# Kernel optimization log

Measured on AMD Instinct MI355X. Metric: run time of the kernel, lower is better.

Reference implementation:

```python
import jax, jax.numpy as jnp
import numpy as np

B, T, T_KEEP, C, F, K = 8, 128, 64, 128, 32, 64


def setup_inputs() -> dict:
    key = jax.random.key(0)
    k1, k2 = jax.random.split(key)
    y_true = jax.random.normal(k1, (B, T, C, F), dtype=jnp.float32)
    # per-timestep mask: 0 = keep, 1 = masked; constant over C,F and batch
    # (required by the original layer's Reshape using sum(1 - masktime[0]))
    masktime = jnp.concatenate([jnp.zeros((T_KEEP,), jnp.float32),
                                jnp.ones((T - T_KEEP,), jnp.float32)])
    mask = jnp.broadcast_to(masktime[None, :, None, None], (B, T, C, F)).astype(jnp.float32)
    centers = jax.random.normal(k2, (K,), dtype=jnp.float32)
    return {"y_true": y_true, "mask": mask, "centers": centers, "t_keep": T_KEEP}


def reference(y_true, mask, centers, t_keep):
    # masktime: [B, T]; mask is constant over channel/feature dims
    masktime = mask[:, :, 0, 0]
    # tf.boolean_mask keeps elements where (1 - mask) is True, preserving order.
    # Since mask is per-timestep, this is a gather of the unmasked timesteps.
    # Stable argsort puts zeros (kept timesteps) first, in original order.
    keep_idx = jnp.argsort(masktime[0], stable=True)[:t_keep]          # [T_keep]
    x = y_true[:, keep_idx]                                            # [B, T_keep, C, F]
    # element-wise nearest-center assignment (assign_center) + one-hot
    dist = jnp.abs(x[..., None] - centers)                             # [B, T_keep, C, F, K]
    idx = jnp.argmin(dist, axis=-1)                                    # [B, T_keep, C, F]
    return jax.nn.one_hot(idx, centers.shape[0], dtype=y_true.dtype)   # [B, T_keep, C, F, K]
```

## Files before the change

### kernel.cpp

```cpp
#include <hip/hip_runtime.h>

constexpr int B = 8, T = 128, T_KEEP = 64, C = 128, F = 32, K = 64;
constexpr int CF = C * F;
constexpr int TOTAL = B * T_KEEP * C * F;
constexpr int BLOCK = 256;
constexpr int EPT = 4;
constexpr int EPB = BLOCK * EPT;

typedef float vfloat4 __attribute__((ext_vector_type(4)));

__global__ void __launch_bounds__(BLOCK) assign_onehot_fused(
        const float* __restrict__ y,
        const float* __restrict__ mask,
        const float* __restrict__ centers,
        float* __restrict__ out) {
    __shared__ float sc[K];
    __shared__ float m_s[T];
    __shared__ int keep_s;
    const int tid = threadIdx.x;

    if (tid < K) sc[tid] = centers[tid];
    if (tid < T) m_s[tid] = mask[(size_t)tid * CF];
    __syncthreads();

    const int t_blk = (blockIdx.x >> 2) & (T_KEEP - 1);
    if (tid < T) {
        float mt = m_s[tid];
        int rank = 0;
        #pragma unroll 8
        for (int j = 0; j < T; ++j) {
            float mj = m_s[j];
            rank += (mj < mt) || (mj == mt && j < tid);
        }
        if (rank == t_blk) keep_s = tid;
    }
    __syncthreads();
    const int keep_t = keep_s;

    const int lane = tid & 63;
    const int wave = tid >> 6;
    const int wbase = blockIdx.x * EPB + wave * (EPT * 64);

    const int b   = wbase >> 18;
    const int cf0 = wbase & (CF - 1);
    const float* ysrc = y + (size_t)b * (T * CF) + (size_t)keep_t * CF + cf0;

    const float x0 = ysrc[lane];
    const float x1 = ysrc[64 + lane];
    const float x2 = ysrc[128 + lane];
    const float x3 = ysrc[192 + lane];

    int bi0 = 0, bi1 = 0, bi2 = 0, bi3 = 0;
    float bd0 = __builtin_inff(), bd1 = bd0, bd2 = bd0, bd3 = bd0;
    const float4* c4 = (const float4*)sc;
    #pragma unroll
    for (int k4 = 0; k4 < K / 4; ++k4) {
        float4 cv = c4[k4];
        float d;
        #define UPD(cvx, kk)                                            \
            d = fabsf(x0 - cvx); if (d < bd0) { bd0 = d; bi0 = kk; }    \
            d = fabsf(x1 - cvx); if (d < bd1) { bd1 = d; bi1 = kk; }    \
            d = fabsf(x2 - cvx); if (d < bd2) { bd2 = d; bi2 = kk; }    \
            d = fabsf(x3 - cvx); if (d < bd3) { bd3 = d; bi3 = kk; }
        UPD(cv.x, 4 * k4 + 0)
        UPD(cv.y, 4 * k4 + 1)
        UPD(cv.z, 4 * k4 + 2)
        UPD(cv.w, 4 * k4 + 3)
        #undef UPD
    }

    vfloat4* out4 = (vfloat4*)out;
    const size_t obase = (size_t)wbase * (K / 4);
    const int k0 = (lane & 15) * 4;
    const int sl_add = lane >> 4;
    #pragma unroll
    for (int i4 = 0; i4 < 64; ++i4) {
        const int e = i4 >> 4;
        int bsel = (e == 0) ? bi0 : (e == 1) ? bi1 : (e == 2) ? bi2 : bi3;
        int bsrc = __shfl(bsel, (i4 & 15) * 4 + sl_add, 64);
        vfloat4 v;
        v.x = (k0 + 0 == bsrc) ? 1.0f : 0.0f;
        v.y = (k0 + 1 == bsrc) ? 1.0f : 0.0f;
        v.z = (k0 + 2 == bsrc) ? 1.0f : 0.0f;
        v.w = (k0 + 3 == bsrc) ? 1.0f : 0.0f;
        __builtin_nontemporal_store(v, &out4[obase + i4 * 64 + lane]);
    }
}

extern "C" void kernel_launch(void* const* d_in, const int* in_sizes, int n_in,
                              void* d_out, int out_size, void* d_ws, size_t ws_size,
                              hipStream_t stream) {
    const float* y       = (const float*)d_in[0];
    const float* mask    = (const float*)d_in[1];
    const float* centers = (const float*)d_in[2];
    float* out = (float*)d_out;

    assign_onehot_fused<<<TOTAL / EPB, BLOCK, 0, stream>>>(y, mask, centers, out);
}
```

Measured before the change: 545.7 us.

## Process full timestep slice per block with prefetch and readlane broadcast

Each block now handles one (batch, kept-timestep) slice of 4096 elements in four chunks instead of 1024 elements. This runs the mask rank computation once per slice rather than once per small block, and prefetches the next chunk's float4 input while the current one is processed. Argmin indices are packed into bytes and broadcast with readlane instead of shfl. The output stores become ordinary stores instead of nontemporal ones, and the grid shrinks to 512 blocks, which may reduce occupancy and latency hiding.

```diff
diff --git a/kernel.cpp b/kernel.cpp
--- a/kernel.cpp
+++ b/kernel.cpp
@@ -2,14 +2,13 @@
 
 constexpr int B = 8, T = 128, T_KEEP = 64, C = 128, F = 32, K = 64;
 constexpr int CF = C * F;
-constexpr int TOTAL = B * T_KEEP * C * F;
 constexpr int BLOCK = 256;
-constexpr int EPT = 4;
-constexpr int EPB = BLOCK * EPT;
+constexpr int CHUNK = 1024;
+constexpr int NCHUNK = CF / CHUNK;
 
 typedef float vfloat4 __attribute__((ext_vector_type(4)));
 
-__global__ void __launch_bounds__(BLOCK) assign_onehot_fused(
+__global__ void __launch_bounds__(BLOCK) assign_onehot_slice(
         const float* __restrict__ y,
         const float* __restrict__ mask,
         const float* __restrict__ centers,
@@ -18,12 +17,14 @@
     __shared__ float m_s[T];
     __shared__ int keep_s;
     const int tid = threadIdx.x;
+    const int bid = blockIdx.x;
+    const int b     = bid >> 6;
+    const int t_blk = bid & (T_KEEP - 1);
 
     if (tid < K) sc[tid] = centers[tid];
     if (tid < T) m_s[tid] = mask[(size_t)tid * CF];
     __syncthreads();
 
-    const int t_blk = (blockIdx.x >> 2) & (T_KEEP - 1);
     if (tid < T) {
         float mt = m_s[tid];
         int rank = 0;
@@ -39,51 +40,55 @@
 
     const int lane = tid & 63;
     const int wave = tid >> 6;
-    const int wbase = blockIdx.x * EPB + wave * (EPT * 64);
 
-    const int b   = wbase >> 18;
-    const int cf0 = wbase & (CF - 1);
-    const float* ysrc = y + (size_t)b * (T * CF) + (size_t)keep_t * CF + cf0;
+    const float4* y4w = (const float4*)(y + (size_t)b * (T * CF)
+                                          + (size_t)keep_t * CF)
+                        + wave * 64 + lane;
 
-    const float x0 = ysrc[lane];
-    const float x1 = ysrc[64 + lane];
-    const float x2 = ysrc[128 + lane];
-    const float x3 = ysrc[192 + lane];
+    vfloat4* ow = (vfloat4*)out
+                + ((size_t)bid * CF + wave * 256) * (K / 4) + lane;
 
-    int bi0 = 0, bi1 = 0, bi2 = 0, bi3 = 0;
-    float bd0 = __builtin_inff(), bd1 = bd0, bd2 = bd0, bd3 = bd0;
+    const int hi = lane >> 4;
+    const int sh = hi * 8;
+    const int k0 = (lane & 15) * 4;
     const float4* c4 = (const float4*)sc;
-    #pragma unroll
-    for (int k4 = 0; k4 < K / 4; ++k4) {
-        float4 cv = c4[k4];
-        float d;
-        #define UPD(cvx, kk)                                            \
-            d = fabsf(x0 - cvx); if (d < bd0) { bd0 = d; bi0 = kk; }    \
-            d = fabsf(x1 - cvx); if (d < bd1) { bd1 = d; bi1 = kk; }    \
-            d = fabsf(x2 - cvx); if (d < bd2) { bd2 = d; bi2 = kk; }    \
-            d = fabsf(x3 - cvx); if (d < bd3) { bd3 = d; bi3 = kk; }
-        UPD(cv.x, 4 * k4 + 0)
-        UPD(cv.y, 4 * k4 + 1)
-        UPD(cv.z, 4 * k4 + 2)
-        UPD(cv.w, 4 * k4 + 3)
-        #undef UPD
-    }
 
-    vfloat4* out4 = (vfloat4*)out;
-    const size_t obase = (size_t)wbase * (K / 4);
-    const int k0 = (lane & 15) * 4;
-    const int sl_add = lane >> 4;
-    #pragma unroll
-    for (int i4 = 0; i4 < 64; ++i4) {
-        const int e = i4 >> 4;
-        int bsel = (e == 0) ? bi0 : (e == 1) ? bi1 : (e == 2) ? bi2 : bi3;
-        int bsrc = __shfl(bsel, (i4 & 15) * 4 + sl_add, 64);
-        vfloat4 v;
-        v.x = (k0 + 0 == bsrc) ? 1.0f : 0.0f;
-        v.y = (k0 + 1 == bsrc) ? 1.0f : 0.0f;
-        v.z = (k0 + 2 == bsrc) ? 1.0f : 0.0f;
-        v.w = (k0 + 3 == bsrc) ? 1.0f : 0.0f;
-        __builtin_nontemporal_store(v, &out4[obase + i4 * 64 + lane]);
+    float4 cur = y4w[0];
+    for (int p = 0; p < NCHUNK; ++p) {
+        float4 nxt = (p + 1 < NCHUNK) ? y4w[(p + 1) * 256] : cur;
+
+        int bi0 = 0, bi1 = 0, bi2 = 0, bi3 = 0;
+        float bd0 = __builtin_inff(), bd1 = bd0, bd2 = bd0, bd3 = bd0;
+        #pragma unroll
+        for (int k4 = 0; k4 < K / 4; ++k4) {
+            float4 cv = c4[k4];
+            float d;
+            #define UPD(cvx, kk)                                            \
+                d = fabsf(cur.x - cvx); if (d < bd0) { bd0 = d; bi0 = kk; } \
+                d = fabsf(cur.y - cvx); if (d < bd1) { bd1 = d; bi1 = kk; } \
+                d = fabsf(cur.z - cvx); if (d < bd2) { bd2 = d; bi2 = kk; } \
+                d = fabsf(cur.w - cvx); if (d < bd3) { bd3 = d; bi3 = kk; }
+            UPD(cv.x, 4 * k4 + 0)
+            UPD(cv.y, 4 * k4 + 1)
+            UPD(cv.z, 4 * k4 + 2)
+            UPD(cv.w, 4 * k4 + 3)
+            #undef UPD
+        }
+        const int packed = bi0 | (bi1 << 8) | (bi2 << 16) | (bi3 << 24);
+
+        vfloat4* op = ow + p * (CHUNK * (K / 4));
+        #pragma unroll
+        for (int i4 = 0; i4 < 64; ++i4) {
+            const int pk   = __builtin_amdgcn_readlane(packed, i4);
+            const int bsrc = (pk >> sh) & 0xff;
+            vfloat4 v;
+            v.x = (bsrc == k0 + 0) ? 1.0f : 0.0f;
+            v.y = (bsrc == k0 + 1) ? 1.0f : 0.0f;
+            v.z = (bsrc == k0 + 2) ? 1.0f : 0.0f;
+            v.w = (bsrc == k0 + 3) ? 1.0f : 0.0f;
+            op[i4 * 64] = v;
+        }
+        cur = nxt;
     }
 }
 
@@ -95,5 +100,5 @@
     const float* centers = (const float*)d_in[2];
     float* out = (float*)d_out;
 
-    assign_onehot_fused<<<TOTAL / EPB, BLOCK, 0, stream>>>(y, mask, centers, out);
+    assign_onehot_slice<<<B * T_KEEP, BLOCK, 0, stream>>>(y, mask, centers, out);
 }
```

New measurement: 545.2 us. No clear change (-0.1%).
